# Kernel tuning notes

Hardware: AMD Instinct MI355X
Metric: run time of the kernel (lower is better)

The kernel has to match this reference:

```python
import jax, jax.numpy as jnp
import numpy as np

N, E, D, H, L = 50000, 800000, 64, 4, 2
DH = D // H


def layer_norm(h, g, b, eps=1e-5):
    mu = h.mean(-1, keepdims=True)
    var = ((h - mu) ** 2).mean(-1, keepdims=True)
    return (h - mu) / jnp.sqrt(var + eps) * g + b


def setup_inputs() -> dict:
    key = jax.random.key(0)
    ks = jax.random.split(key, 16)
    s = 1.0 / np.sqrt(D)
    inp = {
        "x": jax.random.normal(ks[0], (N, D), jnp.float32),
        "edge_attr": jax.random.normal(ks[1], (E, D), jnp.float32),
        "edge_index": jax.random.randint(ks[2], (2, E), 0, N, jnp.int64),
        "WQ": jax.random.normal(ks[3], (L, D, D), jnp.float32) * s,
        "WK": jax.random.normal(ks[4], (L, D, D), jnp.float32) * s,
        "WE": jax.random.normal(ks[5], (L, D, D), jnp.float32) * s,
        "WV": jax.random.normal(ks[6], (L, D, D), jnp.float32) * s,
        "WO": jax.random.normal(ks[7], (L, D, D), jnp.float32) * s,
        "bO": jnp.zeros((L, D), jnp.float32),
        "ln1_g": jnp.ones((L, D), jnp.float32),
        "ln1_b": jnp.zeros((L, D), jnp.float32),
        "W1": jax.random.normal(ks[8], (L, D, 2 * D), jnp.float32) * s,
        "b1": jnp.zeros((L, 2 * D), jnp.float32),
        "W2": jax.random.normal(ks[9], (L, 2 * D, D), jnp.float32) * (1.0 / np.sqrt(2 * D)),
        "b2": jnp.zeros((L, D), jnp.float32),
        "ln2_g": jnp.ones((L, D), jnp.float32),
        "ln2_b": jnp.zeros((L, D), jnp.float32),
    }
    return inp


def exphormer_layer(h, edge_attr, src, dst, p):
    (wq, wk, we, wv, wo, bo, g1, be1, w1, b1, w2, b2, g2, be2) = p
    n = h.shape[0]
    Qh = (h @ wq).reshape(n, H, DH)
    Kh = (h @ wk).reshape(n, H, DH)
    Vh = (h @ wv).reshape(n, H, DH)
    Eh = (edge_attr @ we).reshape(-1, H, DH)
    # per-edge score: sum over head_dim of K[src]*Q[dst]*E / sqrt(DH)
    s = jnp.sum(Kh[src] * Qh[dst] * Eh, axis=-1, keepdims=True) / np.sqrt(DH)
    score = jnp.exp(jnp.clip(s, -5.0, 5.0))  # [E, H, 1]
    msg = Vh[src] * score                     # [E, H, DH]
    wV = jax.ops.segment_sum(msg, dst, num_segments=n)    # [N, H, DH]
    Z = jax.ops.segment_sum(score, dst, num_segments=n)   # [N, H, 1]
    h_attn = (wV / (Z + 1e-6)).reshape(n, D)
    h1 = layer_norm(h + (h_attn @ wo + bo), g1, be1)
    ffn = jax.nn.relu(h1 @ w1 + b1) @ w2 + b2
    return layer_norm(h1 + ffn, g2, be2)


def reference(x, edge_attr, edge_index, WQ, WK, WE, WV, WO, bO, ln1_g, ln1_b,
              W1, b1, W2, b2, ln2_g, ln2_b):
    src = edge_index[0]
    dst = edge_index[1]
    h = x
    for l in range(L):
        p = (WQ[l], WK[l], WE[l], WV[l], WO[l], bO[l], ln1_g[l], ln1_b[l],
             W1[l], b1[l], W2[l], b2[l], ln2_g[l], ln2_b[l])
        h = exphormer_layer(h, edge_attr, src, dst, p)
    return h
```

## Files before the change

kernel.cpp:

```cpp
#include <hip/hip_runtime.h>

#define NN 50000
#define NE 800000
#define D  64
#define NL 2
#define NB 196

typedef __bf16 bf16x8 __attribute__((ext_vector_type(8)));
typedef float  floatx4 __attribute__((ext_vector_type(4)));

static __device__ __forceinline__ float bf2f(unsigned short u) {
    return __uint_as_float(((unsigned)u) << 16);
}
static __device__ __forceinline__ unsigned short f2bf(float x) {
    unsigned u = __float_as_uint(x);
    u += 0x7fff + ((u >> 16) & 1);
    return (unsigned short)(u >> 16);
}


__global__ void k_deg(const int* __restrict__ ei, int* __restrict__ deg) {
    int e = blockIdx.x * 256 + threadIdx.x;
    if (e < NE) atomicAdd(&deg[ei[NE + e]], 1);
}

__global__ __launch_bounds__(256) void k_scan1(const int* __restrict__ deg,
                                               int* __restrict__ psum) {
    __shared__ int red[4];
    int i = blockIdx.x * 256 + threadIdx.x;
    int v = (i < NN) ? deg[i] : 0;
#pragma unroll
    for (int m = 1; m < 64; m <<= 1) v += __shfl_xor(v, m, 64);
    if ((threadIdx.x & 63) == 0) red[threadIdx.x >> 6] = v;
    __syncthreads();
    if (threadIdx.x == 0) psum[blockIdx.x] = red[0] + red[1] + red[2] + red[3];
}

__global__ void k_scan2(int* __restrict__ psum) {
    __shared__ int buf[256];
    int t = threadIdx.x;
    int v = (t < NB) ? psum[t] : 0;
    buf[t] = v;
    __syncthreads();
    for (int o = 1; o < 256; o <<= 1) {
        int x = (t >= o) ? buf[t - o] : 0;
        __syncthreads();
        buf[t] += x;
        __syncthreads();
    }
    if (t < NB) psum[t] = buf[t] - v;
}

__global__ __launch_bounds__(256) void k_scan3(const int* __restrict__ deg,
                                               const int* __restrict__ psum,
                                               int* __restrict__ row_off,
                                               int* __restrict__ cursor) {
    __shared__ int buf[256];
    int t = threadIdx.x;
    int i = blockIdx.x * 256 + t;
    int v = (i < NN) ? deg[i] : 0;
    buf[t] = v;
    __syncthreads();
    for (int o = 1; o < 256; o <<= 1) {
        int x = (t >= o) ? buf[t - o] : 0;
        __syncthreads();
        buf[t] += x;
        __syncthreads();
    }
    if (i < NN) {
        int inc = buf[t] + psum[blockIdx.x];
        row_off[i + 1] = inc;
        cursor[i] = inc - v;
        if (i == 0) row_off[0] = 0;
    }
}

__global__ void k_scatter(const int* __restrict__ ei, int* __restrict__ cursor,
                          int* __restrict__ csr_src, int* __restrict__ csr_dst,
                          int* __restrict__ eperm) {
    int e = blockIdx.x * 256 + threadIdx.x;
    if (e < NE) {
        int dst = ei[NE + e];
        int pos = atomicAdd(&cursor[dst], 1);
        csr_src[pos] = ei[e];
        csr_dst[pos] = dst;
        eperm[e] = pos;
    }
}

__global__ __launch_bounds__(256) void k_prep(
        const float* __restrict__ WQ, const float* __restrict__ WK,
        const float* __restrict__ WV, const float* __restrict__ WE,
        const float* __restrict__ WO, const float* __restrict__ W1,
        const float* __restrict__ W2,
        unsigned short* __restrict__ wqT, unsigned short* __restrict__ wkT,
        unsigned short* __restrict__ wvT, unsigned short* __restrict__ weT,
        unsigned short* __restrict__ woT, unsigned short* __restrict__ w1T,
        unsigned short* __restrict__ w2T) {
    int idx = blockIdx.x * 256 + threadIdx.x;
    if (idx >= 2 * 36864) return;
    int l = idx / 36864;
    int r = idx % 36864;
    if (r < 20480) {
        int which = r >> 12, rr = r & 4095;
        int m = rr >> 6, k = rr & 63;
        const float* src = (which == 0 ? WQ : which == 1 ? WK : which == 2 ? WV :
                            which == 3 ? WE : WO);
        unsigned short* dst = (which == 0 ? wqT : which == 1 ? wkT : which == 2 ? wvT :
                               which == 3 ? weT : woT);
        dst[l * 4096 + rr] = f2bf(src[l * 4096 + k * 64 + m]);
    } else if (r < 28672) {
        int r2 = r - 20480;
        int m = r2 >> 6, k = r2 & 63;
        w1T[l * 8192 + r2] = f2bf(W1[l * 8192 + k * 128 + m]);
    } else {
        int r3 = r - 28672;
        int m = r3 >> 7, k = r3 & 127;
        w2T[l * 8192 + r3] = f2bf(W2[l * 8192 + k * 64 + m]);
    }
}


__global__ __launch_bounds__(256) void k_qkv_mfma(const float* __restrict__ h,
        const unsigned short* __restrict__ wqT, const unsigned short* __restrict__ wkT,
        const unsigned short* __restrict__ wvT,
        float* __restrict__ Qh, unsigned short* __restrict__ Kb,
        unsigned short* __restrict__ Vb) {
    __shared__ unsigned short st[4][16 * 72];
    const int lane = threadIdx.x & 63;
    const int w    = threadIdx.x >> 6;
    const int ml   = lane & 15;
    const int quad = lane >> 4;

    bf16x8 aq[2][4], ak[2][4], av[2][4];
#pragma unroll
    for (int kt = 0; kt < 2; kt++)
#pragma unroll
        for (int mt = 0; mt < 4; mt++) {
            int o = (mt*16 + ml)*64 + kt*32 + quad*8;
            aq[kt][mt] = *(const bf16x8*)&wqT[o];
            ak[kt][mt] = *(const bf16x8*)&wkT[o];
            av[kt][mt] = *(const bf16x8*)&wvT[o];
        }

    const int wave = blockIdx.x * 4 + w;
    const int nw   = gridDim.x * 4;
    for (int tile = wave; tile < NN / 16; tile += nw) {
        const int e0 = tile * 16;
        const float4* ar = (const float4*)(h + (size_t)(e0 + ml) * D);
        bf16x8 b[2];
#pragma unroll
        for (int kt = 0; kt < 2; kt++) {
            float4 f0 = ar[kt*8 + quad*2 + 0];
            float4 f1 = ar[kt*8 + quad*2 + 1];
            b[kt][0] = (__bf16)f0.x; b[kt][1] = (__bf16)f0.y;
            b[kt][2] = (__bf16)f0.z; b[kt][3] = (__bf16)f0.w;
            b[kt][4] = (__bf16)f1.x; b[kt][5] = (__bf16)f1.y;
            b[kt][6] = (__bf16)f1.z; b[kt][7] = (__bf16)f1.w;
        }
        floatx4 accq[4] = {}, acck[4] = {}, accv[4] = {};
#pragma unroll
        for (int kt = 0; kt < 2; kt++)
#pragma unroll
            for (int mt = 0; mt < 4; mt++) {
                accq[mt] = __builtin_amdgcn_mfma_f32_16x16x32_bf16(aq[kt][mt], b[kt], accq[mt], 0, 0, 0);
                acck[mt] = __builtin_amdgcn_mfma_f32_16x16x32_bf16(ak[kt][mt], b[kt], acck[mt], 0, 0, 0);
                accv[mt] = __builtin_amdgcn_mfma_f32_16x16x32_bf16(av[kt][mt], b[kt], accv[mt], 0, 0, 0);
            }
#pragma unroll
        for (int mt = 0; mt < 4; mt++)
            *(float4*)(Qh + (size_t)(e0 + ml) * D + mt*16 + quad*4) =
                make_float4(accq[mt][0], accq[mt][1], accq[mt][2], accq[mt][3]);
        const int el = lane >> 2, c = lane & 3;
#pragma unroll
        for (int mt = 0; mt < 4; mt++)
            *(ushort4*)&st[w][ml*72 + mt*16 + quad*4] =
                make_ushort4(f2bf(acck[mt][0]), f2bf(acck[mt][1]),
                             f2bf(acck[mt][2]), f2bf(acck[mt][3]));
        {
            uint4 r0 = *(const uint4*)&st[w][el*72 + c*16 + 0];
            uint4 r1 = *(const uint4*)&st[w][el*72 + c*16 + 8];
            uint4* gp = (uint4*)(Kb + (size_t)(e0 + el) * D + c*16);
            gp[0] = r0; gp[1] = r1;
        }
#pragma unroll
        for (int mt = 0; mt < 4; mt++)
            *(ushort4*)&st[w][ml*72 + mt*16 + quad*4] =
                make_ushort4(f2bf(accv[mt][0]), f2bf(accv[mt][1]),
                             f2bf(accv[mt][2]), f2bf(accv[mt][3]));
        {
            uint4 r0 = *(const uint4*)&st[w][el*72 + c*16 + 0];
            uint4 r1 = *(const uint4*)&st[w][el*72 + c*16 + 8];
            uint4* gp = (uint4*)(Vb + (size_t)(e0 + el) * D + c*16);
            gp[0] = r0; gp[1] = r1;
        }
    }
}

__global__ __launch_bounds__(256) void k_eh_score(const float* __restrict__ ea,
        const unsigned short* __restrict__ weT, const int* __restrict__ eperm,
        const int* __restrict__ ei, const float* __restrict__ Qh,
        const unsigned short* __restrict__ Kb,
        float* __restrict__ scb, unsigned short* __restrict__ Eh1) {
    __shared__ unsigned short st[4][16 * 72];
    const int lane = threadIdx.x & 63;
    const int w    = threadIdx.x >> 6;
    const int ml   = lane & 15;
    const int quad = lane >> 4;

    bf16x8 afr[2][2][4];
#pragma unroll
    for (int l = 0; l < 2; l++)
#pragma unroll
        for (int kt = 0; kt < 2; kt++)
#pragma unroll
            for (int mt = 0; mt < 4; mt++)
                afr[l][kt][mt] = *(const bf16x8*)&weT[l*4096 + (mt*16 + ml)*64 + kt*32 + quad*8];

    const int wave = blockIdx.x * 4 + w;
    const int nw   = gridDim.x * 4;
    const int el = lane >> 2, c = lane & 3;
    for (int tile = wave; tile < NE / 16; tile += nw) {
        const int e0 = tile * 16;
        const float4* ar = (const float4*)(ea + (size_t)(e0 + ml) * D);
        bf16x8 b[2];
#pragma unroll
        for (int kt = 0; kt < 2; kt++) {
            float4 f0 = ar[kt*8 + quad*2 + 0];
            float4 f1 = ar[kt*8 + quad*2 + 1];
            b[kt][0] = (__bf16)f0.x; b[kt][1] = (__bf16)f0.y;
            b[kt][2] = (__bf16)f0.z; b[kt][3] = (__bf16)f0.w;
            b[kt][4] = (__bf16)f1.x; b[kt][5] = (__bf16)f1.y;
            b[kt][6] = (__bf16)f1.z; b[kt][7] = (__bf16)f1.w;
        }
        const int eid  = e0 + ml;
        const int srcn = ei[eid];
        const int dstn = ei[NE + eid];
        const int posm = eperm[eid];
        const int pose = eperm[e0 + el];

        {
            floatx4 acc[4] = {};
#pragma unroll
            for (int kt = 0; kt < 2; kt++)
#pragma unroll
                for (int mt = 0; mt < 4; mt++)
                    acc[mt] = __builtin_amdgcn_mfma_f32_16x16x32_bf16(afr[0][kt][mt], b[kt], acc[mt], 0, 0, 0);
            float scq[4];
#pragma unroll
            for (int mt = 0; mt < 4; mt++) {
                float4 q4 = *(const float4*)(Qh + (size_t)dstn * D + mt*16 + quad*4);
                ushort4 k4 = *(const ushort4*)(Kb + (size_t)srcn * D + mt*16 + quad*4);
                float p = acc[mt][0] * q4.x * bf2f(k4.x)
                        + acc[mt][1] * q4.y * bf2f(k4.y)
                        + acc[mt][2] * q4.z * bf2f(k4.z)
                        + acc[mt][3] * q4.w * bf2f(k4.w);
                p += __shfl_xor(p, 16, 64);
                p += __shfl_xor(p, 32, 64);
                scq[mt] = __expf(fminf(5.f, fmaxf(-5.f, p * 0.25f)));
            }
            if (quad == 0)
                *(float4*)(scb + (size_t)posm * 4) =
                    make_float4(scq[0], scq[1], scq[2], scq[3]);
        }
        {
            floatx4 acc[4] = {};
#pragma unroll
            for (int kt = 0; kt < 2; kt++)
#pragma unroll
                for (int mt = 0; mt < 4; mt++)
                    acc[mt] = __builtin_amdgcn_mfma_f32_16x16x32_bf16(afr[1][kt][mt], b[kt], acc[mt], 0, 0, 0);
#pragma unroll
            for (int mt = 0; mt < 4; mt++)
                *(ushort4*)&st[w][ml*72 + mt*16 + quad*4] =
                    make_ushort4(f2bf(acc[mt][0]), f2bf(acc[mt][1]),
                                 f2bf(acc[mt][2]), f2bf(acc[mt][3]));
            uint4 r0 = *(const uint4*)&st[w][el*72 + c*16 + 0];
            uint4 r1 = *(const uint4*)&st[w][el*72 + c*16 + 8];
            uint4* gp = (uint4*)(Eh1 + (size_t)pose * D + c*16);
            gp[0] = r0;
            gp[1] = r1;
        }
    }
}

__global__ __launch_bounds__(256) void k_score1(
        const unsigned short* __restrict__ Eh1,
        const float* __restrict__ Qh, const unsigned short* __restrict__ Kb,
        const int* __restrict__ csr_src, const int* __restrict__ csr_dst,
        float* __restrict__ scb) {
    const int lane = threadIdx.x & 63;
    const int w    = threadIdx.x >> 6;
    const int ml   = lane & 15;
    const int quad = lane >> 4;
    const int wave = blockIdx.x * 4 + w;
    const int nw   = gridDim.x * 4;
    for (int tile = wave; tile < NE / 16; tile += nw) {
        const int p = tile * 16 + ml;
        const int src = csr_src[p];
        const int dst = csr_dst[p];
        bf16x8 e0v = *(const bf16x8*)(Eh1 + (size_t)p * D + quad*16);
        bf16x8 e1v = *(const bf16x8*)(Eh1 + (size_t)p * D + quad*16 + 8);
        bf16x8 k0v = *(const bf16x8*)(Kb + (size_t)src * D + quad*16);
        bf16x8 k1v = *(const bf16x8*)(Kb + (size_t)src * D + quad*16 + 8);
        const float4* qp = (const float4*)(Qh + (size_t)dst * D + quad*16);
        float4 q0 = qp[0], q1 = qp[1], q2 = qp[2], q3 = qp[3];
        float s = (float)e0v[0] * q0.x * (float)k0v[0]
                + (float)e0v[1] * q0.y * (float)k0v[1]
                + (float)e0v[2] * q0.z * (float)k0v[2]
                + (float)e0v[3] * q0.w * (float)k0v[3]
                + (float)e0v[4] * q1.x * (float)k0v[4]
                + (float)e0v[5] * q1.y * (float)k0v[5]
                + (float)e0v[6] * q1.z * (float)k0v[6]
                + (float)e0v[7] * q1.w * (float)k0v[7]
                + (float)e1v[0] * q2.x * (float)k1v[0]
                + (float)e1v[1] * q2.y * (float)k1v[1]
                + (float)e1v[2] * q2.z * (float)k1v[2]
                + (float)e1v[3] * q2.w * (float)k1v[3]
                + (float)e1v[4] * q3.x * (float)k1v[4]
                + (float)e1v[5] * q3.y * (float)k1v[5]
                + (float)e1v[6] * q3.z * (float)k1v[6]
                + (float)e1v[7] * q3.w * (float)k1v[7];
        scb[(size_t)p * 4 + quad] = __expf(fminf(5.f, fmaxf(-5.f, s * 0.25f)));
    }
}

__global__ __launch_bounds__(256) void k_agg(
        const unsigned short* __restrict__ Vb, const float* __restrict__ scb,
        const int* __restrict__ row_off, const int* __restrict__ csr_src,
        float* __restrict__ h_attn) {
    const int node = blockIdx.x * 4 + (threadIdx.x >> 6);
    if (node >= NN) return;
    const int lane  = threadIdx.x & 63;
    const int eslot = lane >> 4;
    const int ml    = lane & 15;
    const int hsel  = ml >> 2;
    const int beg = row_off[node], end = row_off[node + 1];
    float4 acc = make_float4(0.f, 0.f, 0.f, 0.f);
    float z = 0.f;

    for (int cbeg = beg; cbeg < end; cbeg += 64) {
        const int cnt = min(64, end - cbeg);
        int myidx = cbeg + lane;
        int mysrc = (myidx < end) ? csr_src[myidx] : 0;

        for (int base = 0; base < cnt; base += 16) {
            int  jj[4];
            int  s[4];
            bool act[4];
#pragma unroll
            for (int u = 0; u < 4; u++) {
                int j = base + eslot + 4 * u;
                act[u] = j < cnt;
                jj[u]  = act[u] ? j : 0;
                s[u]   = __shfl(mysrc, jj[u], 64);
            }
            ushort4 vb[4];
            float   sv[4];
#pragma unroll
            for (int u = 0; u < 4; u++) {
                vb[u] = *(const ushort4*)(Vb + (size_t)s[u] * D + ml * 4);
                sv[u] = scb[(size_t)(cbeg + jj[u]) * 4 + hsel];
            }
#pragma unroll
            for (int u = 0; u < 4; u++) {
                float sc = act[u] ? sv[u] : 0.f;
                acc.x += sc * bf2f(vb[u].x);
                acc.y += sc * bf2f(vb[u].y);
                acc.z += sc * bf2f(vb[u].z);
                acc.w += sc * bf2f(vb[u].w);
                z += sc;
            }
        }
    }
#pragma unroll
    for (int m = 16; m <= 32; m <<= 1) {
        acc.x += __shfl_xor(acc.x, m, 64);
        acc.y += __shfl_xor(acc.y, m, 64);
        acc.z += __shfl_xor(acc.z, m, 64);
        acc.w += __shfl_xor(acc.w, m, 64);
        z     += __shfl_xor(z, m, 64);
    }
    if (eslot == 0) {
        float inv = 1.f / (z + 1e-6f);
        ((float4*)(h_attn + (size_t)node * D))[ml] =
            make_float4(acc.x * inv, acc.y * inv, acc.z * inv, acc.w * inv);
    }
}

__global__ __launch_bounds__(512) void k_post_mfma(const float* __restrict__ h_in,
        const float* __restrict__ h_attn,
        const unsigned short* __restrict__ woT_g,
        const unsigned short* __restrict__ w1T_g,
        const unsigned short* __restrict__ w2T_g,
        const float* __restrict__ bo,
        const float* __restrict__ g1, const float* __restrict__ be1,
        const float* __restrict__ b1, const float* __restrict__ b2,
        const float* __restrict__ g2, const float* __restrict__ be2,
        float* __restrict__ h_out) {
    __shared__ unsigned short woT_s[64 * 72];
    __shared__ unsigned short w1T_s[128 * 72];
    __shared__ unsigned short w2T_s[64 * 136];
    __shared__ unsigned short stg[8][16 * 136];

    const int t = threadIdx.x;
    {
        const uint4* s0 = (const uint4*)woT_g;
        { int i = t; if (i < 512) { int row = i >> 3, c = i & 7;
              *(uint4*)&woT_s[row*72 + c*8] = s0[i]; } }
        const uint4* s1 = (const uint4*)w1T_g;
        for (int i = t; i < 1024; i += 512) {
            int row = i >> 3, c = i & 7;
            *(uint4*)&w1T_s[row*72 + c*8] = s1[i];
        }
        const uint4* s2 = (const uint4*)w2T_g;
        for (int i = t; i < 1024; i += 512) {
            int row = i >> 4, c = i & 15;
            *(uint4*)&w2T_s[row*136 + c*8] = s2[i];
        }
    }
    __syncthreads();

    const int w = t >> 6, lane = t & 63;
    const int ml = lane & 15, quad = lane >> 4;
    const int tile = blockIdx.x * 8 + w;
    if (tile >= NN / 16) return;
    const int e0 = tile * 16;
    unsigned short* st = stg[w];

    const float4* ap = (const float4*)(h_attn + (size_t)(e0 + ml) * D);
    floatx4 acc1[4] = {};
#pragma unroll
    for (int kt = 0; kt < 2; kt++) {
        float4 f0 = ap[kt*8 + quad*2 + 0];
        float4 f1 = ap[kt*8 + quad*2 + 1];
        bf16x8 b;
        b[0] = (__bf16)f0.x; b[1] = (__bf16)f0.y; b[2] = (__bf16)f0.z; b[3] = (__bf16)f0.w;
        b[4] = (__bf16)f1.x; b[5] = (__bf16)f1.y; b[6] = (__bf16)f1.z; b[7] = (__bf16)f1.w;
#pragma unroll
        for (int mt = 0; mt < 4; mt++) {
            bf16x8 a = *(const bf16x8*)&woT_s[(mt*16 + ml)*72 + kt*32 + quad*8];
            acc1[mt] = __builtin_amdgcn_mfma_f32_16x16x32_bf16(a, b, acc1[mt], 0, 0, 0);
        }
    }
    const float4* hp  = (const float4*)(h_in + (size_t)(e0 + ml) * D);
    const float4* bo4 = (const float4*)bo;
    floatx4 tt[4];
#pragma unroll
    for (int mt = 0; mt < 4; mt++) {
        float4 hh = hp[mt*4 + quad];
        float4 bb = bo4[mt*4 + quad];
        tt[mt][0] = acc1[mt][0] + hh.x + bb.x;
        tt[mt][1] = acc1[mt][1] + hh.y + bb.y;
        tt[mt][2] = acc1[mt][2] + hh.z + bb.z;
        tt[mt][3] = acc1[mt][3] + hh.w + bb.w;
    }
    float s = 0.f;
#pragma unroll
    for (int mt = 0; mt < 4; mt++) s += tt[mt][0] + tt[mt][1] + tt[mt][2] + tt[mt][3];
    s += __shfl_xor(s, 16, 64); s += __shfl_xor(s, 32, 64);
    float mu = s * (1.f / 64.f);
    float v = 0.f;
#pragma unroll
    for (int mt = 0; mt < 4; mt++)
#pragma unroll
        for (int r = 0; r < 4; r++) { float c = tt[mt][r] - mu; v += c * c; }
    v += __shfl_xor(v, 16, 64); v += __shfl_xor(v, 32, 64);
    float rstd = rsqrtf(v * (1.f / 64.f) + 1e-5f);
    const float4* g1v  = (const float4*)g1;
    const float4* be1v = (const float4*)be1;
    floatx4 h1[4];
#pragma unroll
    for (int mt = 0; mt < 4; mt++) {
        float4 gg = g1v[mt*4 + quad];
        float4 bb = be1v[mt*4 + quad];
        h1[mt][0] = (tt[mt][0] - mu) * rstd * gg.x + bb.x;
        h1[mt][1] = (tt[mt][1] - mu) * rstd * gg.y + bb.y;
        h1[mt][2] = (tt[mt][2] - mu) * rstd * gg.z + bb.z;
        h1[mt][3] = (tt[mt][3] - mu) * rstd * gg.w + bb.w;
        *(ushort4*)&st[ml*136 + mt*16 + quad*4] =
            make_ushort4(f2bf(h1[mt][0]), f2bf(h1[mt][1]), f2bf(h1[mt][2]), f2bf(h1[mt][3]));
    }

    bf16x8 bh[2];
#pragma unroll
    for (int kt = 0; kt < 2; kt++)
        bh[kt] = *(const bf16x8*)&st[ml*136 + kt*32 + quad*8];
    floatx4 acc2[8] = {};
#pragma unroll
    for (int kt = 0; kt < 2; kt++)
#pragma unroll
        for (int mt = 0; mt < 8; mt++) {
            bf16x8 a = *(const bf16x8*)&w1T_s[(mt*16 + ml)*72 + kt*32 + quad*8];
            acc2[mt] = __builtin_amdgcn_mfma_f32_16x16x32_bf16(a, bh[kt], acc2[mt], 0, 0, 0);
        }
    const float4* b1v = (const float4*)b1;
#pragma unroll
    for (int mt = 0; mt < 8; mt++) {
        float4 bb = b1v[mt*4 + quad];
        float y0 = fmaxf(acc2[mt][0] + bb.x, 0.f);
        float y1 = fmaxf(acc2[mt][1] + bb.y, 0.f);
        float y2 = fmaxf(acc2[mt][2] + bb.z, 0.f);
        float y3 = fmaxf(acc2[mt][3] + bb.w, 0.f);
        *(ushort4*)&st[ml*136 + mt*16 + quad*4] =
            make_ushort4(f2bf(y0), f2bf(y1), f2bf(y2), f2bf(y3));
    }

    floatx4 acc3[4] = {};
#pragma unroll
    for (int kt = 0; kt < 4; kt++) {
        bf16x8 b = *(const bf16x8*)&st[ml*136 + kt*32 + quad*8];
#pragma unroll
        for (int mt = 0; mt < 4; mt++) {
            bf16x8 a = *(const bf16x8*)&w2T_s[(mt*16 + ml)*136 + kt*32 + quad*8];
            acc3[mt] = __builtin_amdgcn_mfma_f32_16x16x32_bf16(a, b, acc3[mt], 0, 0, 0);
        }
    }
    const float4* b2v = (const float4*)b2;
#pragma unroll
    for (int mt = 0; mt < 4; mt++) {
        float4 bb = b2v[mt*4 + quad];
        tt[mt][0] = acc3[mt][0] + bb.x + h1[mt][0];
        tt[mt][1] = acc3[mt][1] + bb.y + h1[mt][1];
        tt[mt][2] = acc3[mt][2] + bb.z + h1[mt][2];
        tt[mt][3] = acc3[mt][3] + bb.w + h1[mt][3];
    }
    s = 0.f;
#pragma unroll
    for (int mt = 0; mt < 4; mt++) s += tt[mt][0] + tt[mt][1] + tt[mt][2] + tt[mt][3];
    s += __shfl_xor(s, 16, 64); s += __shfl_xor(s, 32, 64);
    mu = s * (1.f / 64.f);
    v = 0.f;
#pragma unroll
    for (int mt = 0; mt < 4; mt++)
#pragma unroll
        for (int r = 0; r < 4; r++) { float c = tt[mt][r] - mu; v += c * c; }
    v += __shfl_xor(v, 16, 64); v += __shfl_xor(v, 32, 64);
    rstd = rsqrtf(v * (1.f / 64.f) + 1e-5f);
    const float4* g2v  = (const float4*)g2;
    const float4* be2v = (const float4*)be2;
    float4* outp = (float4*)(h_out + (size_t)(e0 + ml) * D);
#pragma unroll
    for (int mt = 0; mt < 4; mt++) {
        float4 gg = g2v[mt*4 + quad];
        float4 bb = be2v[mt*4 + quad];
        float4 o;
        o.x = (tt[mt][0] - mu) * rstd * gg.x + bb.x;
        o.y = (tt[mt][1] - mu) * rstd * gg.y + bb.y;
        o.z = (tt[mt][2] - mu) * rstd * gg.z + bb.z;
        o.w = (tt[mt][3] - mu) * rstd * gg.w + bb.w;
        outp[mt*4 + quad] = o;
    }
}


extern "C" void kernel_launch(void* const* d_in, const int* in_sizes, int n_in,
                              void* d_out, int out_size, void* d_ws, size_t ws_size,
                              hipStream_t stream) {
    const float* x   = (const float*)d_in[0];
    const float* ea  = (const float*)d_in[1];
    const int*   ei  = (const int*)d_in[2];
    const float* WQ  = (const float*)d_in[3];
    const float* WK  = (const float*)d_in[4];
    const float* WE  = (const float*)d_in[5];
    const float* WV  = (const float*)d_in[6];
    const float* WO  = (const float*)d_in[7];
    const float* bO  = (const float*)d_in[8];
    const float* g1  = (const float*)d_in[9];
    const float* be1 = (const float*)d_in[10];
    const float* W1  = (const float*)d_in[11];
    const float* b1  = (const float*)d_in[12];
    const float* W2  = (const float*)d_in[13];
    const float* b2  = (const float*)d_in[14];
    const float* g2  = (const float*)d_in[15];
    const float* be2 = (const float*)d_in[16];
    float* out = (float*)d_out;

    char* wsb = (char*)d_ws;
    size_t off = 0;
    auto alloc = [&](size_t bytes) {
        void* p = wsb + off;
        off += (bytes + 255) & ~(size_t)255;
        return p;
    };
    float* Qh            = (float*)alloc((size_t)NN * D * 4);
    unsigned short* Kb   = (unsigned short*)alloc((size_t)NN * D * 2);
    unsigned short* Vb   = (unsigned short*)alloc((size_t)NN * D * 2);
    float* hbuf          = (float*)alloc((size_t)NN * D * 4);
    float* hattn         = (float*)alloc((size_t)NN * D * 4);
    unsigned short* Eh1  = (unsigned short*)alloc((size_t)NE * D * 2);
    float* scb           = (float*)alloc((size_t)NE * 4 * 4);
    int* row_off         = (int*)alloc((size_t)(NN + 1) * 4);
    int* cursor          = (int*)alloc((size_t)NN * 4);
    int* deg             = (int*)alloc((size_t)NN * 4);
    int* psum            = (int*)alloc((size_t)256 * 4);
    int* csr_src         = (int*)alloc((size_t)NE * 4);
    int* csr_dst         = (int*)alloc((size_t)NE * 4);
    int* eperm           = (int*)alloc((size_t)NE * 4);
    unsigned short* wqT  = (unsigned short*)alloc((size_t)2 * 4096 * 2);
    unsigned short* wkT  = (unsigned short*)alloc((size_t)2 * 4096 * 2);
    unsigned short* wvT  = (unsigned short*)alloc((size_t)2 * 4096 * 2);
    unsigned short* weT  = (unsigned short*)alloc((size_t)2 * 4096 * 2);
    unsigned short* woT  = (unsigned short*)alloc((size_t)2 * 4096 * 2);
    unsigned short* w1T  = (unsigned short*)alloc((size_t)2 * 8192 * 2);
    unsigned short* w2T  = (unsigned short*)alloc((size_t)2 * 8192 * 2);

    hipMemsetAsync(deg, 0, (size_t)NN * 4, stream);
    k_deg<<<(NE + 255) / 256, 256, 0, stream>>>(ei, deg);
    k_scan1<<<NB, 256, 0, stream>>>(deg, psum);
    k_scan2<<<1, 256, 0, stream>>>(psum);
    k_scan3<<<NB, 256, 0, stream>>>(deg, psum, row_off, cursor);
    k_scatter<<<(NE + 255) / 256, 256, 0, stream>>>(ei, cursor, csr_src, csr_dst, eperm);
    k_prep<<<(2 * 36864 + 255) / 256, 256, 0, stream>>>(WQ, WK, WV, WE, WO, W1, W2,
            wqT, wkT, wvT, weT, woT, w1T, w2T);

    k_qkv_mfma<<<782, 256, 0, stream>>>(x, wqT, wkT, wvT, Qh, Kb, Vb);
    k_eh_score<<<1536, 256, 0, stream>>>(ea, weT, eperm, ei, Qh, Kb, scb, Eh1);

    k_agg<<<(NN + 3) / 4, 256, 0, stream>>>(Vb, scb, row_off, csr_src, hattn);
    k_post_mfma<<<(NN / 16 + 7) / 8, 512, 0, stream>>>(x, hattn,
            woT, w1T, w2T, bO, g1, be1, b1, b2, g2, be2, hbuf);

    k_qkv_mfma<<<782, 256, 0, stream>>>(hbuf, wqT + 4096, wkT + 4096,
                                        wvT + 4096, Qh, Kb, Vb);
    k_score1<<<1536, 256, 0, stream>>>(Eh1, Qh, Kb, csr_src, csr_dst, scb);
    k_agg<<<(NN + 3) / 4, 256, 0, stream>>>(Vb, scb, row_off, csr_src, hattn);
    k_post_mfma<<<(NN / 16 + 7) / 8, 512, 0, stream>>>(hbuf, hattn,
            woT + 4096, w1T + 8192, w2T + 8192,
            bO + 64, g1 + 64, be1 + 64, b1 + 128, b2 + 64,
            g2 + 64, be2 + 64, out);
}
```

Baseline: 619.6 us.

## Store Q in bf16, stage edge weights in LDS, and prefetch gather indices

Q is now written as bf16 through the same LDS transpose path used for K and V, halving the bytes of the per-edge Q gathers in both score kernels. The edge-score kernel keeps the WE weights in shared memory instead of registers, issues the Q/K gathers early, and prefetches the next tile's indices. It also reorders the Eh1 write ahead of the score computation. The second-layer score kernel gets the same software prefetch of CSR indices and Eh1. This adds some Q precision loss from bf16 rounding and extra LDS traffic for the weight fragments.

```diff
diff --git a/kernel.cpp b/kernel.cpp
--- a/kernel.cpp
+++ b/kernel.cpp
@@ -124,7 +124,7 @@
 __global__ __launch_bounds__(256) void k_qkv_mfma(const float* __restrict__ h,
         const unsigned short* __restrict__ wqT, const unsigned short* __restrict__ wkT,
         const unsigned short* __restrict__ wvT,
-        float* __restrict__ Qh, unsigned short* __restrict__ Kb,
+        unsigned short* __restrict__ Qb, unsigned short* __restrict__ Kb,
         unsigned short* __restrict__ Vb) {
     __shared__ unsigned short st[4][16 * 72];
     const int lane = threadIdx.x & 63;
@@ -145,6 +145,7 @@
 
     const int wave = blockIdx.x * 4 + w;
     const int nw   = gridDim.x * 4;
+    const int el = lane >> 2, c = lane & 3;
     for (int tile = wave; tile < NN / 16; tile += nw) {
         const int e0 = tile * 16;
         const float4* ar = (const float4*)(h + (size_t)(e0 + ml) * D);
@@ -169,9 +170,15 @@
             }
 #pragma unroll
         for (int mt = 0; mt < 4; mt++)
-            *(float4*)(Qh + (size_t)(e0 + ml) * D + mt*16 + quad*4) =
-                make_float4(accq[mt][0], accq[mt][1], accq[mt][2], accq[mt][3]);
-        const int el = lane >> 2, c = lane & 3;
+            *(ushort4*)&st[w][ml*72 + mt*16 + quad*4] =
+                make_ushort4(f2bf(accq[mt][0]), f2bf(accq[mt][1]),
+                             f2bf(accq[mt][2]), f2bf(accq[mt][3]));
+        {
+            uint4 r0 = *(const uint4*)&st[w][el*72 + c*16 + 0];
+            uint4 r1 = *(const uint4*)&st[w][el*72 + c*16 + 8];
+            uint4* gp = (uint4*)(Qb + (size_t)(e0 + el) * D + c*16);
+            gp[0] = r0; gp[1] = r1;
+        }
 #pragma unroll
         for (int mt = 0; mt < 4; mt++)
             *(ushort4*)&st[w][ml*72 + mt*16 + quad*4] =
@@ -199,77 +206,73 @@
 
 __global__ __launch_bounds__(256) void k_eh_score(const float* __restrict__ ea,
         const unsigned short* __restrict__ weT, const int* __restrict__ eperm,
-        const int* __restrict__ ei, const float* __restrict__ Qh,
+        const int* __restrict__ ei, const unsigned short* __restrict__ Qb,
         const unsigned short* __restrict__ Kb,
         float* __restrict__ scb, unsigned short* __restrict__ Eh1) {
+    __shared__ unsigned short wsm[2 * 4608];
     __shared__ unsigned short st[4][16 * 72];
-    const int lane = threadIdx.x & 63;
-    const int w    = threadIdx.x >> 6;
+    const int t = threadIdx.x;
+    for (int i = t; i < 1024; i += 256) {
+        int l = i >> 9, r = i & 511;
+        *(uint4*)&wsm[l*4608 + (r >> 3)*72 + (r & 7)*8] = ((const uint4*)weT)[i];
+    }
+    __syncthreads();
+
+    const int lane = t & 63;
+    const int w    = t >> 6;
     const int ml   = lane & 15;
     const int quad = lane >> 4;
-
-    bf16x8 afr[2][2][4];
-#pragma unroll
-    for (int l = 0; l < 2; l++)
-#pragma unroll
-        for (int kt = 0; kt < 2; kt++)
-#pragma unroll
-            for (int mt = 0; mt < 4; mt++)
-                afr[l][kt][mt] = *(const bf16x8*)&weT[l*4096 + (mt*16 + ml)*64 + kt*32 + quad*8];
-
+    const int el = lane >> 2, c = lane & 3;
     const int wave = blockIdx.x * 4 + w;
     const int nw   = gridDim.x * 4;
-    const int el = lane >> 2, c = lane & 3;
-    for (int tile = wave; tile < NE / 16; tile += nw) {
-        const int e0 = tile * 16;
-        const float4* ar = (const float4*)(ea + (size_t)(e0 + ml) * D);
+    const int NT   = NE / 16;
+
+    int tile = wave;
+    if (tile >= NT) return;
+    int srcn = ei[tile*16 + ml];
+    int dstn = ei[NE + tile*16 + ml];
+    int posm = eperm[tile*16 + ml];
+    int pose = eperm[tile*16 + el];
+
+    for (; tile < NT; tile += nw) {
+        const float4* ar = (const float4*)(ea + (size_t)(tile*16 + ml) * D);
+        float4 f00 = ar[quad*2 + 0];
+        float4 f01 = ar[quad*2 + 1];
+        float4 f10 = ar[8 + quad*2 + 0];
+        float4 f11 = ar[8 + quad*2 + 1];
+        ushort4 qg[4], kg[4];
+#pragma unroll
+        for (int mt = 0; mt < 4; mt++) {
+            qg[mt] = *(const ushort4*)(Qb + (size_t)dstn * D + mt*16 + quad*4);
+            kg[mt] = *(const ushort4*)(Kb + (size_t)srcn * D + mt*16 + quad*4);
+        }
+        int nxt = tile + nw;
+        int nsrc = srcn, ndst = dstn, nposm = posm, npose = pose;
+        if (nxt < NT) {
+            nsrc  = ei[nxt*16 + ml];
+            ndst  = ei[NE + nxt*16 + ml];
+            nposm = eperm[nxt*16 + ml];
+            npose = eperm[nxt*16 + el];
+        }
         bf16x8 b[2];
-#pragma unroll
-        for (int kt = 0; kt < 2; kt++) {
-            float4 f0 = ar[kt*8 + quad*2 + 0];
-            float4 f1 = ar[kt*8 + quad*2 + 1];
-            b[kt][0] = (__bf16)f0.x; b[kt][1] = (__bf16)f0.y;
-            b[kt][2] = (__bf16)f0.z; b[kt][3] = (__bf16)f0.w;
-            b[kt][4] = (__bf16)f1.x; b[kt][5] = (__bf16)f1.y;
-            b[kt][6] = (__bf16)f1.z; b[kt][7] = (__bf16)f1.w;
-        }
-        const int eid  = e0 + ml;
-        const int srcn = ei[eid];
-        const int dstn = ei[NE + eid];
-        const int posm = eperm[eid];
-        const int pose = eperm[e0 + el];
+        b[0][0] = (__bf16)f00.x; b[0][1] = (__bf16)f00.y;
+        b[0][2] = (__bf16)f00.z; b[0][3] = (__bf16)f00.w;
+        b[0][4] = (__bf16)f01.x; b[0][5] = (__bf16)f01.y;
+        b[0][6] = (__bf16)f01.z; b[0][7] = (__bf16)f01.w;
+        b[1][0] = (__bf16)f10.x; b[1][1] = (__bf16)f10.y;
+        b[1][2] = (__bf16)f10.z; b[1][3] = (__bf16)f10.w;
+        b[1][4] = (__bf16)f11.x; b[1][5] = (__bf16)f11.y;
+        b[1][6] = (__bf16)f11.z; b[1][7] = (__bf16)f11.w;
 
         {
             floatx4 acc[4] = {};
 #pragma unroll
             for (int kt = 0; kt < 2; kt++)
 #pragma unroll
-                for (int mt = 0; mt < 4; mt++)
-                    acc[mt] = __builtin_amdgcn_mfma_f32_16x16x32_bf16(afr[0][kt][mt], b[kt], acc[mt], 0, 0, 0);
-            float scq[4];
-#pragma unroll
-            for (int mt = 0; mt < 4; mt++) {
-                float4 q4 = *(const float4*)(Qh + (size_t)dstn * D + mt*16 + quad*4);
-                ushort4 k4 = *(const ushort4*)(Kb + (size_t)srcn * D + mt*16 + quad*4);
-                float p = acc[mt][0] * q4.x * bf2f(k4.x)
-                        + acc[mt][1] * q4.y * bf2f(k4.y)
-                        + acc[mt][2] * q4.z * bf2f(k4.z)
-                        + acc[mt][3] * q4.w * bf2f(k4.w);
-                p += __shfl_xor(p, 16, 64);
-                p += __shfl_xor(p, 32, 64);
-                scq[mt] = __expf(fminf(5.f, fmaxf(-5.f, p * 0.25f)));
-            }
-            if (quad == 0)
-                *(float4*)(scb + (size_t)posm * 4) =
-                    make_float4(scq[0], scq[1], scq[2], scq[3]);
-        }
-        {
-            floatx4 acc[4] = {};
-#pragma unroll
-            for (int kt = 0; kt < 2; kt++)
-#pragma unroll
-                for (int mt = 0; mt < 4; mt++)
-                    acc[mt] = __builtin_amdgcn_mfma_f32_16x16x32_bf16(afr[1][kt][mt], b[kt], acc[mt], 0, 0, 0);
+                for (int mt = 0; mt < 4; mt++) {
+                    bf16x8 a = *(const bf16x8*)&wsm[4608 + (mt*16 + ml)*72 + kt*32 + quad*8];
+                    acc[mt] = __builtin_amdgcn_mfma_f32_16x16x32_bf16(a, b[kt], acc[mt], 0, 0, 0);
+                }
 #pragma unroll
             for (int mt = 0; mt < 4; mt++)
                 *(ushort4*)&st[w][ml*72 + mt*16 + quad*4] =
@@ -281,12 +284,37 @@
             gp[0] = r0;
             gp[1] = r1;
         }
+        {
+            floatx4 acc[4] = {};
+#pragma unroll
+            for (int kt = 0; kt < 2; kt++)
+#pragma unroll
+                for (int mt = 0; mt < 4; mt++) {
+                    bf16x8 a = *(const bf16x8*)&wsm[(mt*16 + ml)*72 + kt*32 + quad*8];
+                    acc[mt] = __builtin_amdgcn_mfma_f32_16x16x32_bf16(a, b[kt], acc[mt], 0, 0, 0);
+                }
+            float scq[4];
+#pragma unroll
+            for (int mt = 0; mt < 4; mt++) {
+                float p = acc[mt][0] * bf2f(qg[mt].x) * bf2f(kg[mt].x)
+                        + acc[mt][1] * bf2f(qg[mt].y) * bf2f(kg[mt].y)
+                        + acc[mt][2] * bf2f(qg[mt].z) * bf2f(kg[mt].z)
+                        + acc[mt][3] * bf2f(qg[mt].w) * bf2f(kg[mt].w);
+                p += __shfl_xor(p, 16, 64);
+                p += __shfl_xor(p, 32, 64);
+                scq[mt] = __expf(fminf(5.f, fmaxf(-5.f, p * 0.25f)));
+            }
+            if (quad == 0)
+                *(float4*)(scb + (size_t)posm * 4) =
+                    make_float4(scq[0], scq[1], scq[2], scq[3]);
+        }
+        srcn = nsrc; dstn = ndst; posm = nposm; pose = npose;
     }
 }
 
 __global__ __launch_bounds__(256) void k_score1(
         const unsigned short* __restrict__ Eh1,
-        const float* __restrict__ Qh, const unsigned short* __restrict__ Kb,
+        const unsigned short* __restrict__ Qb, const unsigned short* __restrict__ Kb,
         const int* __restrict__ csr_src, const int* __restrict__ csr_dst,
         float* __restrict__ scb) {
     const int lane = threadIdx.x & 63;
@@ -295,33 +323,34 @@
     const int quad = lane >> 4;
     const int wave = blockIdx.x * 4 + w;
     const int nw   = gridDim.x * 4;
-    for (int tile = wave; tile < NE / 16; tile += nw) {
-        const int p = tile * 16 + ml;
-        const int src = csr_src[p];
-        const int dst = csr_dst[p];
-        bf16x8 e0v = *(const bf16x8*)(Eh1 + (size_t)p * D + quad*16);
-        bf16x8 e1v = *(const bf16x8*)(Eh1 + (size_t)p * D + quad*16 + 8);
-        bf16x8 k0v = *(const bf16x8*)(Kb + (size_t)src * D + quad*16);
-        bf16x8 k1v = *(const bf16x8*)(Kb + (size_t)src * D + quad*16 + 8);
-        const float4* qp = (const float4*)(Qh + (size_t)dst * D + quad*16);
-        float4 q0 = qp[0], q1 = qp[1], q2 = qp[2], q3 = qp[3];
-        float s = (float)e0v[0] * q0.x * (float)k0v[0]
-                + (float)e0v[1] * q0.y * (float)k0v[1]
-                + (float)e0v[2] * q0.z * (float)k0v[2]
-                + (float)e0v[3] * q0.w * (float)k0v[3]
-                + (float)e0v[4] * q1.x * (float)k0v[4]
-                + (float)e0v[5] * q1.y * (float)k0v[5]
-                + (float)e0v[6] * q1.z * (float)k0v[6]
-                + (float)e0v[7] * q1.w * (float)k0v[7]
-                + (float)e1v[0] * q2.x * (float)k1v[0]
-                + (float)e1v[1] * q2.y * (float)k1v[1]
-                + (float)e1v[2] * q2.z * (float)k1v[2]
-                + (float)e1v[3] * q2.w * (float)k1v[3]
-                + (float)e1v[4] * q3.x * (float)k1v[4]
-                + (float)e1v[5] * q3.y * (float)k1v[5]
-                + (float)e1v[6] * q3.z * (float)k1v[6]
-                + (float)e1v[7] * q3.w * (float)k1v[7];
-        scb[(size_t)p * 4 + quad] = __expf(fminf(5.f, fmaxf(-5.f, s * 0.25f)));
+    const int NT   = NE / 16;
+    int tile = wave;
+    if (tile >= NT) return;
+    int p0 = tile*16 + ml;
+    int src = csr_src[p0], dst = csr_dst[p0];
+    bf16x8 e0 = *(const bf16x8*)(Eh1 + (size_t)p0 * D + quad*16);
+    bf16x8 e1 = *(const bf16x8*)(Eh1 + (size_t)p0 * D + quad*16 + 8);
+    for (; tile < NT; tile += nw) {
+        bf16x8 k0 = *(const bf16x8*)(Kb + (size_t)src * D + quad*16);
+        bf16x8 k1 = *(const bf16x8*)(Kb + (size_t)src * D + quad*16 + 8);
+        bf16x8 q0 = *(const bf16x8*)(Qb + (size_t)dst * D + quad*16);
+        bf16x8 q1 = *(const bf16x8*)(Qb + (size_t)dst * D + quad*16 + 8);
+        int nxt = tile + nw;
+        int nsrc = src, ndst = dst;
+        bf16x8 ne0 = e0, ne1 = e1;
+        if (nxt < NT) {
+            int pn = nxt*16 + ml;
+            nsrc = csr_src[pn]; ndst = csr_dst[pn];
+            ne0 = *(const bf16x8*)(Eh1 + (size_t)pn * D + quad*16);
+            ne1 = *(const bf16x8*)(Eh1 + (size_t)pn * D + quad*16 + 8);
+        }
+        float s = 0.f;
+#pragma unroll
+        for (int i = 0; i < 8; i++) s += (float)e0[i] * (float)q0[i] * (float)k0[i];
+#pragma unroll
+        for (int i = 0; i < 8; i++) s += (float)e1[i] * (float)q1[i] * (float)k1[i];
+        scb[(size_t)(tile*16 + ml) * 4 + quad] = __expf(fminf(5.f, fmaxf(-5.f, s * 0.25f)));
+        src = nsrc; dst = ndst; e0 = ne0; e1 = ne1;
     }
 }
 
@@ -583,7 +612,7 @@
         off += (bytes + 255) & ~(size_t)255;
         return p;
     };
-    float* Qh            = (float*)alloc((size_t)NN * D * 4);
+    unsigned short* Qb   = (unsigned short*)alloc((size_t)NN * D * 2);
     unsigned short* Kb   = (unsigned short*)alloc((size_t)NN * D * 2);
     unsigned short* Vb   = (unsigned short*)alloc((size_t)NN * D * 2);
     float* hbuf          = (float*)alloc((size_t)NN * D * 4);
@@ -614,16 +643,16 @@
     k_prep<<<(2 * 36864 + 255) / 256, 256, 0, stream>>>(WQ, WK, WV, WE, WO, W1, W2,
             wqT, wkT, wvT, weT, woT, w1T, w2T);
 
-    k_qkv_mfma<<<782, 256, 0, stream>>>(x, wqT, wkT, wvT, Qh, Kb, Vb);
-    k_eh_score<<<1536, 256, 0, stream>>>(ea, weT, eperm, ei, Qh, Kb, scb, Eh1);
+    k_qkv_mfma<<<782, 256, 0, stream>>>(x, wqT, wkT, wvT, Qb, Kb, Vb);
+    k_eh_score<<<1280, 256, 0, stream>>>(ea, weT, eperm, ei, Qb, Kb, scb, Eh1);
 
     k_agg<<<(NN + 3) / 4, 256, 0, stream>>>(Vb, scb, row_off, csr_src, hattn);
     k_post_mfma<<<(NN / 16 + 7) / 8, 512, 0, stream>>>(x, hattn,
             woT, w1T, w2T, bO, g1, be1, b1, b2, g2, be2, hbuf);
 
     k_qkv_mfma<<<782, 256, 0, stream>>>(hbuf, wqT + 4096, wkT + 4096,
-                                        wvT + 4096, Qh, Kb, Vb);
-    k_score1<<<1536, 256, 0, stream>>>(Eh1, Qh, Kb, csr_src, csr_dst, scb);
+                                        wvT + 4096, Qb, Kb, Vb);
+    k_score1<<<1536, 256, 0, stream>>>(Eh1, Qb, Kb, csr_src, csr_dst, scb);
     k_agg<<<(NN + 3) / 4, 256, 0, stream>>>(Vb, scb, row_off, csr_src, hattn);
     k_post_mfma<<<(NN / 16 + 7) / 8, 512, 0, stream>>>(hbuf, hattn,
             woT + 4096, w1T + 8192, w2T + 8192,
```

Measured after the change: 605.8 us. 1.02x faster.
